# Kernel optimization log

Hardware: AMD Instinct MI355X
Metric: run time of the kernel (lower is better)

The kernel has to match this reference:

```python
import jax, jax.numpy as jnp
import numpy as np

N = 100000   # nodes
E = 1600000  # edges
F_IN = 256   # input features
H = 64       # hidden
C = 40       # classes


def setup_inputs() -> dict:
    key = jax.random.key(0)
    k = jax.random.split(key, 5)
    x = jax.random.normal(k[0], (N, F_IN), dtype=jnp.float32)
    edge_index = jax.random.randint(k[1], (2, E), 0, N, dtype=jnp.int64)
    edge_attr = jax.random.uniform(k[2], (E,), dtype=jnp.float32)
    # GCNConv params (glorot-ish scale), biases zero like reset_parameters
    W1 = jax.random.normal(k[3], (F_IN, H), dtype=jnp.float32) * (1.0 / np.sqrt(F_IN))
    b1 = jnp.zeros((H,), dtype=jnp.float32)
    W2 = jax.random.normal(k[4], (H, C), dtype=jnp.float32) * (1.0 / np.sqrt(H))
    b2 = jnp.zeros((C,), dtype=jnp.float32)
    return {"x": x, "edge_index": edge_index, "edge_attr": edge_attr,
            "W1": W1, "b1": b1, "W2": W2, "b2": b2}


def _gcn_conv(x, W, b, src, dst, norm):
    h = x @ W                                   # [N, out]
    msg = h[src] * norm[:, None]                # gather + edge scale [E+N, out]
    out = jax.ops.segment_sum(msg, dst, num_segments=N)
    return out + b


def reference(x, edge_index, edge_attr, W1, b1, W2, b2):
    # gcn_norm: add self-loops (weight 1), symmetric D^-1/2 A D^-1/2
    loop = jnp.arange(N, dtype=edge_index.dtype)
    src = jnp.concatenate([edge_index[0], loop])
    dst = jnp.concatenate([edge_index[1], loop])
    w = jnp.concatenate([edge_attr, jnp.ones((N,), dtype=edge_attr.dtype)])
    deg = jax.ops.segment_sum(w, dst, num_segments=N)
    dinv = jnp.where(deg > 0, jax.lax.rsqrt(jnp.maximum(deg, 1e-30)), 0.0)
    norm = dinv[src] * w * dinv[dst]

    h = _gcn_conv(x, W1, b1, src, dst, norm)
    h = jax.nn.relu(h)                          # dropout is identity in eval mode
    h = _gcn_conv(h, W2, b2, src, dst, norm)
    return jax.nn.log_softmax(h, axis=1)
```

## Files before the change

### kernel.cpp

```cpp
#include <hip/hip_runtime.h>
#include <math.h>

#define NN   100000
#define NE   1600000
#define FIN  256
#define HID  64
#define NC   40
#define NBKT 391
#define EPB  6250
#define CAP  4608

typedef __attribute__((ext_vector_type(8))) short short8;
typedef __attribute__((ext_vector_type(4))) float float4v;

static __device__ __forceinline__ short f2bf(float f) {
    unsigned u = __float_as_uint(f);
    u += 0x7FFFu + ((u >> 16) & 1u);
    return (short)(u >> 16);
}
static __device__ __forceinline__ float bf2f(unsigned short b) {
    return __uint_as_float((unsigned)b << 16);
}

__global__ __launch_bounds__(256) void w1cvt_k(const float* __restrict__ W1,
                                               short* __restrict__ w1t) {
    int t = blockIdx.x * 256 + threadIdx.x;
    int k = t >> 6, n = t & 63;
    w1t[n * FIN + k] = f2bf(W1[k * HID + n]);
}

__global__ __launch_bounds__(256) void phaseA_k(const int* __restrict__ src,
                                                const int* __restrict__ dst,
                                                const float* __restrict__ w,
                                                int* __restrict__ cursor,
                                                int2* __restrict__ bucketbuf) {
    __shared__ int  hist[NBKT];
    __shared__ int  sc[512];
    __shared__ int  loc_base[NBKT];
    __shared__ int  loc_cur[NBKT];
    __shared__ int  gb[NBKT];
    __shared__ int2 buf[EPB];
    const int t  = threadIdx.x;
    const int e0 = blockIdx.x * EPB;

    for (int i = t; i < NBKT; i += 256) hist[i] = 0;
    __syncthreads();
    for (int i = t; i < EPB; i += 256) atomicAdd(&hist[dst[e0 + i] >> 8], 1);
    __syncthreads();
    sc[t]       = (t       < NBKT) ? hist[t]       : 0;
    sc[t + 256] = (t + 256 < NBKT) ? hist[t + 256] : 0;
    __syncthreads();
    for (int off = 1; off < 512; off <<= 1) {
        int a0 = (t >= off) ? sc[t - off] : 0;
        int a1 = sc[t + 256 - off];
        __syncthreads();
        sc[t] += a0; sc[t + 256] += a1;
        __syncthreads();
    }
    for (int i = t; i < NBKT; i += 256) {
        int base = sc[i] - hist[i];
        loc_base[i] = base;
        loc_cur[i]  = base;
        gb[i] = atomicAdd(&cursor[i * 16], hist[i]);
    }
    __syncthreads();
    for (int i = t; i < EPB; i += 256) {
        int e = e0 + i;
        int d = dst[e];
        int b = d >> 8;
        int p = atomicAdd(&loc_cur[b], 1);
        buf[p] = make_int2(src[e] | ((d & 255) << 17), __float_as_int(w[e]));
    }
    __syncthreads();
    for (int b = t; b < NBKT; b += 256) {
        int lb = loc_base[b], n = hist[b];
        int2* dstp = bucketbuf + (size_t)b * CAP + gb[b];
        for (int i = 0; i < n; ++i) dstp[i] = buf[lb + i];
    }
}

__global__ __launch_bounds__(512) void scanB_k(const int* __restrict__ cursor,
                                               int* __restrict__ bucketbase,
                                               int* __restrict__ row_start) {
    __shared__ int tmp[512];
    int t = threadIdx.x;
    int v = (t < NBKT) ? cursor[t * 16] : 0;
    tmp[t] = v;
    __syncthreads();
    for (int off = 1; off < 512; off <<= 1) {
        int add = (t >= off) ? tmp[t - off] : 0;
        __syncthreads(); tmp[t] += add; __syncthreads();
    }
    if (t < NBKT) bucketbase[t] = tmp[t] - v;
    if (t == 0) { bucketbase[NBKT] = NE; row_start[NN] = NE; }
}

__global__ __launch_bounds__(256) void phaseB_k(const int* __restrict__ bucketbase,
                                                const int2* __restrict__ bucketbuf,
                                                int2* __restrict__ e8,
                                                int* __restrict__ row_start,
                                                float* __restrict__ dinv) {
    __shared__ int2 buf[CAP];
    __shared__ int2 buf2[CAP];
    __shared__ int  hist2[256];
    __shared__ int  tmp[256];
    __shared__ int  base2[257];
    __shared__ int  cur2[256];
    const int b = blockIdx.x, t = threadIdx.x;
    const int g0   = bucketbase[b];
    const int cntb = bucketbase[b + 1] - g0;
    const int n0   = b * 256;
    const int nnb  = (NN - n0 < 256) ? (NN - n0) : 256;

    hist2[t] = 0;
    __syncthreads();
    const int2* bb = bucketbuf + (size_t)b * CAP;
    for (int i = t; i < cntb; i += 256) {
        int2 kv = bb[i];
        buf[i] = kv;
        atomicAdd(&hist2[kv.x >> 17], 1);
    }
    __syncthreads();
    int v = hist2[t];
    tmp[t] = v;
    __syncthreads();
    for (int off = 1; off < 256; off <<= 1) {
        int add = (t >= off) ? tmp[t - off] : 0;
        __syncthreads(); tmp[t] += add; __syncthreads();
    }
    int excl = tmp[t] - v;
    base2[t] = excl;
    cur2[t]  = excl;
    if (t == 0) base2[256] = cntb;
    if (t < nnb) row_start[n0 + t] = g0 + excl;
    __syncthreads();
    for (int i = t; i < cntb; i += 256) {
        int2 kv = buf[i];
        int d = kv.x >> 17;
        int p = atomicAdd(&cur2[d], 1);
        buf2[p] = make_int2(kv.x & 0x1FFFF, kv.y);
    }
    __syncthreads();
    for (int i = t; i < cntb; i += 256) e8[g0 + i] = buf2[i];
    if (t < nnb) {
        float s = 0.f;
        int j1 = base2[t + 1];
        for (int j = base2[t]; j < j1; ++j) s += __int_as_float(buf2[j].y);
        dinv[n0 + t] = rsqrtf(1.0f + s);
    }
}

__global__ __launch_bounds__(256) void gemm1_mfma_k(const float* __restrict__ x,
                                                    const short* __restrict__ w1t,
                                                    unsigned short* __restrict__ h1) {
    const int wave = threadIdx.x >> 6;
    const int lane = threadIdx.x & 63;
    const int m    = lane & 15;
    const int quad = lane >> 4;
    const int r0   = blockIdx.x * 64 + wave * 16;
    const int row  = r0 + m;
    const int rcl  = (row < NN) ? row : (NN - 1);
    const float* xrow = x + (size_t)rcl * FIN + quad * 8;

    float4v acc0 = {0.f,0.f,0.f,0.f}, acc1 = acc0, acc2 = acc0, acc3 = acc0;

#pragma unroll
    for (int kc = 0; kc < 8; ++kc) {
        const int kof = kc * 32 + quad * 8;
        float4 xa = *(const float4*)(xrow + kc * 32);
        float4 xb = *(const float4*)(xrow + kc * 32 + 4);
        short8 a;
        a[0] = f2bf(xa.x); a[1] = f2bf(xa.y); a[2] = f2bf(xa.z); a[3] = f2bf(xa.w);
        a[4] = f2bf(xb.x); a[5] = f2bf(xb.y); a[6] = f2bf(xb.z); a[7] = f2bf(xb.w);
        short8 b0 = *(const short8*)(w1t + (0 * 16 + m) * FIN + kof);
        short8 b1 = *(const short8*)(w1t + (1 * 16 + m) * FIN + kof);
        short8 b2 = *(const short8*)(w1t + (2 * 16 + m) * FIN + kof);
        short8 b3 = *(const short8*)(w1t + (3 * 16 + m) * FIN + kof);
        acc0 = __builtin_amdgcn_mfma_f32_16x16x32_bf16(a, b0, acc0, 0, 0, 0);
        acc1 = __builtin_amdgcn_mfma_f32_16x16x32_bf16(a, b1, acc1, 0, 0, 0);
        acc2 = __builtin_amdgcn_mfma_f32_16x16x32_bf16(a, b2, acc2, 0, 0, 0);
        acc3 = __builtin_amdgcn_mfma_f32_16x16x32_bf16(a, b3, acc3, 0, 0, 0);
    }
#pragma unroll
    for (int r = 0; r < 4; ++r) {
        int rr = r0 + quad * 4 + r;
        if (rr < NN) {
            unsigned short* hp = h1 + (size_t)rr * HID + m;
            hp[0]  = (unsigned short)f2bf(acc0[r]);
            hp[16] = (unsigned short)f2bf(acc1[r]);
            hp[32] = (unsigned short)f2bf(acc2[r]);
            hp[48] = (unsigned short)f2bf(acc3[r]);
        }
    }
}

__global__ __launch_bounds__(256) void gather64_k(const int* __restrict__ row_start,
                                                  const int2* __restrict__ e8,
                                                  const float* __restrict__ dinv,
                                                  const unsigned short* __restrict__ h,
                                                  float* __restrict__ agg) {
    const int v = blockIdx.x * 4 + (threadIdx.x >> 6);
    const int lane = threadIdx.x & 63;
    const int i0 = row_start[v], i1 = row_start[v + 1];
    float acc0 = 0.f, acc1 = 0.f, acc2 = 0.f, acc3 = 0.f;
    int i = i0;
    for (; i + 4 <= i1; i += 4) {
        int2 a = e8[i + 0], b = e8[i + 1], c = e8[i + 2], d = e8[i + 3];
        float wa = dinv[a.x] * __int_as_float(a.y);
        float wb = dinv[b.x] * __int_as_float(b.y);
        float wc = dinv[c.x] * __int_as_float(c.y);
        float wd = dinv[d.x] * __int_as_float(d.y);
        acc0 = fmaf(bf2f(h[(size_t)a.x * HID + lane]), wa, acc0);
        acc1 = fmaf(bf2f(h[(size_t)b.x * HID + lane]), wb, acc1);
        acc2 = fmaf(bf2f(h[(size_t)c.x * HID + lane]), wc, acc2);
        acc3 = fmaf(bf2f(h[(size_t)d.x * HID + lane]), wd, acc3);
    }
    for (; i < i1; ++i) {
        int2 a = e8[i];
        acc0 = fmaf(bf2f(h[(size_t)a.x * HID + lane]), dinv[a.x] * __int_as_float(a.y), acc0);
    }
    const float dv = dinv[v];
    float r = dv * ((acc0 + acc1) + (acc2 + acc3));
    r = fmaf(dv * dv, bf2f(h[(size_t)v * HID + lane]), r);
    agg[(size_t)v * HID + lane] = r;
}

__global__ __launch_bounds__(256) void gemm2_k(const float* __restrict__ agg1,
                                               const float* __restrict__ b1,
                                               const float* __restrict__ W2,
                                               unsigned short* __restrict__ h2) {
    __shared__ float w2s[HID * NC];
    __shared__ float b1s[HID];
    for (int i = threadIdx.x; i < HID * NC; i += 256) w2s[i] = W2[i];
    if (threadIdx.x < HID) b1s[threadIdx.x] = b1[threadIdx.x];
    __syncthreads();

    const int r = blockIdx.x * 256 + threadIdx.x;
    if (r >= NN) return;
    float acc[NC];
#pragma unroll
    for (int c = 0; c < NC; ++c) acc[c] = 0.f;

    const float4* row4 = (const float4*)(agg1 + (size_t)r * HID);
    for (int kk = 0; kk < HID; kk += 4) {
        float4 v = row4[kk >> 2];
        float xr0 = fmaxf(v.x + b1s[kk + 0], 0.f);
        float xr1 = fmaxf(v.y + b1s[kk + 1], 0.f);
        float xr2 = fmaxf(v.z + b1s[kk + 2], 0.f);
        float xr3 = fmaxf(v.w + b1s[kk + 3], 0.f);
#pragma unroll
        for (int c = 0; c < NC; ++c) {
            acc[c] = fmaf(xr0, w2s[(kk + 0) * NC + c], acc[c]);
            acc[c] = fmaf(xr1, w2s[(kk + 1) * NC + c], acc[c]);
            acc[c] = fmaf(xr2, w2s[(kk + 2) * NC + c], acc[c]);
            acc[c] = fmaf(xr3, w2s[(kk + 3) * NC + c], acc[c]);
        }
    }
    unsigned short* outp = h2 + (size_t)r * NC;
    ushort2* o2 = (ushort2*)outp;
#pragma unroll
    for (int c = 0; c < NC; c += 2)
        o2[c >> 1] = make_ushort2((unsigned short)f2bf(acc[c]), (unsigned short)f2bf(acc[c + 1]));
}

__global__ __launch_bounds__(256) void gather40_logsm_k(const int* __restrict__ row_start,
                                                        const int2* __restrict__ e8,
                                                        const float* __restrict__ dinv,
                                                        const unsigned short* __restrict__ h,
                                                        const float* __restrict__ b2,
                                                        float* __restrict__ out) {
    const int v = blockIdx.x * 4 + (threadIdx.x >> 6);
    const int lane = threadIdx.x & 63;
    const int i0 = row_start[v], i1 = row_start[v + 1];
    const int cl = (lane < NC) ? lane : 0;
    float acc0 = 0.f, acc1 = 0.f, acc2 = 0.f, acc3 = 0.f;
    int i = i0;
    for (; i + 4 <= i1; i += 4) {
        int2 a = e8[i + 0], b = e8[i + 1], c = e8[i + 2], d = e8[i + 3];
        float wa = dinv[a.x] * __int_as_float(a.y);
        float wb = dinv[b.x] * __int_as_float(b.y);
        float wc = dinv[c.x] * __int_as_float(c.y);
        float wd = dinv[d.x] * __int_as_float(d.y);
        acc0 = fmaf(bf2f(h[(size_t)a.x * NC + cl]), wa, acc0);
        acc1 = fmaf(bf2f(h[(size_t)b.x * NC + cl]), wb, acc1);
        acc2 = fmaf(bf2f(h[(size_t)c.x * NC + cl]), wc, acc2);
        acc3 = fmaf(bf2f(h[(size_t)d.x * NC + cl]), wd, acc3);
    }
    for (; i < i1; ++i) {
        int2 a = e8[i];
        acc0 = fmaf(bf2f(h[(size_t)a.x * NC + cl]), dinv[a.x] * __int_as_float(a.y), acc0);
    }
    const float dv = dinv[v];
    float vv = dv * ((acc0 + acc1) + (acc2 + acc3));
    vv = fmaf(dv * dv, bf2f(h[(size_t)v * NC + cl]), vv);
    vv += b2[cl];

    float m = (lane < NC) ? vv : -INFINITY;
#pragma unroll
    for (int off = 32; off >= 1; off >>= 1) m = fmaxf(m, __shfl_xor(m, off, 64));
    float ex = (lane < NC) ? __expf(vv - m) : 0.f;
    float s = ex;
#pragma unroll
    for (int off = 32; off >= 1; off >>= 1) s += __shfl_xor(s, off, 64);
    if (lane < NC) out[(size_t)v * NC + lane] = vv - m - __logf(s);
}

extern "C" void kernel_launch(void* const* d_in, const int* in_sizes, int n_in,
                              void* d_out, int out_size, void* d_ws, size_t ws_size,
                              hipStream_t stream) {
    const float* x  = (const float*)d_in[0];
    const int*   ei = (const int*)d_in[1];
    const float* ea = (const float*)d_in[2];
    const float* W1 = (const float*)d_in[3];
    const float* b1 = (const float*)d_in[4];
    const float* W2 = (const float*)d_in[5];
    const float* b2 = (const float*)d_in[6];
    const int* src = ei;
    const int* dst = ei + NE;
    float* out = (float*)d_out;

    char* ws = (char*)d_ws;
    float* dinv       = (float*)(ws + 0);
    int*   row_start  = (int*)  (ws + 400000);
    int*   cursor     = (int*)  (ws + 800016);
    int*   bucketbase = (int*)  (ws + 825040);
    int2*  e8         = (int2*) (ws + 826608);
    unsigned short* h1 = (unsigned short*)(ws + 13626608);
    float* agg1       = (float*)(ws + 26426608);
    short* w1t        = (short*)(ws + 52026608);
    int2*  bucketbuf  = (int2*)agg1;
    unsigned short* h2 = h1;

    hipMemsetAsync(cursor, 0, 391 * 16 * sizeof(int), stream);

    w1cvt_k <<<64,   256, 0, stream>>>(W1, w1t);
    phaseA_k<<<256,  256, 0, stream>>>(src, dst, ea, cursor, bucketbuf);
    scanB_k <<<1,    512, 0, stream>>>(cursor, bucketbase, row_start);
    phaseB_k<<<NBKT, 256, 0, stream>>>(bucketbase, bucketbuf, e8, row_start, dinv);

    gemm1_mfma_k    <<<(NN + 63) / 64, 256, 0, stream>>>(x, w1t, h1);
    gather64_k      <<<NN / 4, 256, 0, stream>>>(row_start, e8, dinv, h1, agg1);
    gemm2_k         <<<(NN + 255) / 256, 256, 0, stream>>>(agg1, b1, W2, h2);
    gather40_logsm_k<<<NN / 4, 256, 0, stream>>>(row_start, e8, dinv, h2, b2, out);
}
```

Before: 431.6 us.

## Pre-scale features by dinv and aggregate before second GEMM

Folds the source-side D^-1/2 scaling into the producer kernels (GEMM1 output and post-ReLU activations), so the edge loops no longer gather dinv per edge. Reorders layer 2 to aggregate the 64-wide hidden features first and then multiply by W2, fusing bias and log-softmax into a per-row GEMM kernel. This removes a random dinv gather per edge in both passes and the separate gemm2 kernel. In exchange the second gather reads 64-wide rows instead of 40-wide ones, writes a float agg2 buffer, and adds a per-thread softmax over 40 registers.

```diff
diff --git a/kernel.cpp b/kernel.cpp
--- a/kernel.cpp
+++ b/kernel.cpp
@@ -152,6 +152,7 @@
 
 __global__ __launch_bounds__(256) void gemm1_mfma_k(const float* __restrict__ x,
                                                     const short* __restrict__ w1t,
+                                                    const float* __restrict__ dinv,
                                                     unsigned short* __restrict__ h1) {
     const int wave = threadIdx.x >> 6;
     const int lane = threadIdx.x & 63;
@@ -185,20 +186,22 @@
     for (int r = 0; r < 4; ++r) {
         int rr = r0 + quad * 4 + r;
         if (rr < NN) {
+            float dv = dinv[rr];
             unsigned short* hp = h1 + (size_t)rr * HID + m;
-            hp[0]  = (unsigned short)f2bf(acc0[r]);
-            hp[16] = (unsigned short)f2bf(acc1[r]);
-            hp[32] = (unsigned short)f2bf(acc2[r]);
-            hp[48] = (unsigned short)f2bf(acc3[r]);
+            hp[0]  = (unsigned short)f2bf(acc0[r] * dv);
+            hp[16] = (unsigned short)f2bf(acc1[r] * dv);
+            hp[32] = (unsigned short)f2bf(acc2[r] * dv);
+            hp[48] = (unsigned short)f2bf(acc3[r] * dv);
         }
     }
 }
 
-__global__ __launch_bounds__(256) void gather64_k(const int* __restrict__ row_start,
-                                                  const int2* __restrict__ e8,
-                                                  const float* __restrict__ dinv,
-                                                  const unsigned short* __restrict__ h,
-                                                  float* __restrict__ agg) {
+__global__ __launch_bounds__(256) void gatherA_k(const int* __restrict__ row_start,
+                                                 const int2* __restrict__ e8,
+                                                 const float* __restrict__ dinv,
+                                                 const unsigned short* __restrict__ h,
+                                                 const float* __restrict__ b1,
+                                                 unsigned short* __restrict__ Rp) {
     const int v = blockIdx.x * 4 + (threadIdx.x >> 6);
     const int lane = threadIdx.x & 63;
     const int i0 = row_start[v], i1 = row_start[v + 1];
@@ -206,103 +209,86 @@
     int i = i0;
     for (; i + 4 <= i1; i += 4) {
         int2 a = e8[i + 0], b = e8[i + 1], c = e8[i + 2], d = e8[i + 3];
-        float wa = dinv[a.x] * __int_as_float(a.y);
-        float wb = dinv[b.x] * __int_as_float(b.y);
-        float wc = dinv[c.x] * __int_as_float(c.y);
-        float wd = dinv[d.x] * __int_as_float(d.y);
-        acc0 = fmaf(bf2f(h[(size_t)a.x * HID + lane]), wa, acc0);
-        acc1 = fmaf(bf2f(h[(size_t)b.x * HID + lane]), wb, acc1);
-        acc2 = fmaf(bf2f(h[(size_t)c.x * HID + lane]), wc, acc2);
-        acc3 = fmaf(bf2f(h[(size_t)d.x * HID + lane]), wd, acc3);
+        acc0 = fmaf(bf2f(h[(size_t)a.x * HID + lane]), __int_as_float(a.y), acc0);
+        acc1 = fmaf(bf2f(h[(size_t)b.x * HID + lane]), __int_as_float(b.y), acc1);
+        acc2 = fmaf(bf2f(h[(size_t)c.x * HID + lane]), __int_as_float(c.y), acc2);
+        acc3 = fmaf(bf2f(h[(size_t)d.x * HID + lane]), __int_as_float(d.y), acc3);
     }
     for (; i < i1; ++i) {
         int2 a = e8[i];
-        acc0 = fmaf(bf2f(h[(size_t)a.x * HID + lane]), dinv[a.x] * __int_as_float(a.y), acc0);
+        acc0 = fmaf(bf2f(h[(size_t)a.x * HID + lane]), __int_as_float(a.y), acc0);
     }
     const float dv = dinv[v];
-    float r = dv * ((acc0 + acc1) + (acc2 + acc3));
-    r = fmaf(dv * dv, bf2f(h[(size_t)v * HID + lane]), r);
-    agg[(size_t)v * HID + lane] = r;
-}
-
-__global__ __launch_bounds__(256) void gemm2_k(const float* __restrict__ agg1,
-                                               const float* __restrict__ b1,
-                                               const float* __restrict__ W2,
-                                               unsigned short* __restrict__ h2) {
-    __shared__ float w2s[HID * NC];
-    __shared__ float b1s[HID];
-    for (int i = threadIdx.x; i < HID * NC; i += 256) w2s[i] = W2[i];
-    if (threadIdx.x < HID) b1s[threadIdx.x] = b1[threadIdx.x];
-    __syncthreads();
-
-    const int r = blockIdx.x * 256 + threadIdx.x;
-    if (r >= NN) return;
-    float acc[NC];
-#pragma unroll
-    for (int c = 0; c < NC; ++c) acc[c] = 0.f;
-
-    const float4* row4 = (const float4*)(agg1 + (size_t)r * HID);
-    for (int kk = 0; kk < HID; kk += 4) {
-        float4 v = row4[kk >> 2];
-        float xr0 = fmaxf(v.x + b1s[kk + 0], 0.f);
-        float xr1 = fmaxf(v.y + b1s[kk + 1], 0.f);
-        float xr2 = fmaxf(v.z + b1s[kk + 2], 0.f);
-        float xr3 = fmaxf(v.w + b1s[kk + 3], 0.f);
-#pragma unroll
-        for (int c = 0; c < NC; ++c) {
-            acc[c] = fmaf(xr0, w2s[(kk + 0) * NC + c], acc[c]);
-            acc[c] = fmaf(xr1, w2s[(kk + 1) * NC + c], acc[c]);
-            acc[c] = fmaf(xr2, w2s[(kk + 2) * NC + c], acc[c]);
-            acc[c] = fmaf(xr3, w2s[(kk + 3) * NC + c], acc[c]);
-        }
-    }
-    unsigned short* outp = h2 + (size_t)r * NC;
-    ushort2* o2 = (ushort2*)outp;
-#pragma unroll
-    for (int c = 0; c < NC; c += 2)
-        o2[c >> 1] = make_ushort2((unsigned short)f2bf(acc[c]), (unsigned short)f2bf(acc[c + 1]));
-}
-
-__global__ __launch_bounds__(256) void gather40_logsm_k(const int* __restrict__ row_start,
-                                                        const int2* __restrict__ e8,
-                                                        const float* __restrict__ dinv,
-                                                        const unsigned short* __restrict__ h,
-                                                        const float* __restrict__ b2,
-                                                        float* __restrict__ out) {
+    float r = (acc0 + acc1) + (acc2 + acc3);
+    r = dv * (r + bf2f(h[(size_t)v * HID + lane]));
+    r = fmaxf(r + b1[lane], 0.f);
+    Rp[(size_t)v * HID + lane] = (unsigned short)f2bf(dv * r);
+}
+
+__global__ __launch_bounds__(256) void gatherB_k(const int* __restrict__ row_start,
+                                                 const int2* __restrict__ e8,
+                                                 const float* __restrict__ dinv,
+                                                 const unsigned short* __restrict__ Rp,
+                                                 float* __restrict__ agg2) {
     const int v = blockIdx.x * 4 + (threadIdx.x >> 6);
     const int lane = threadIdx.x & 63;
     const int i0 = row_start[v], i1 = row_start[v + 1];
-    const int cl = (lane < NC) ? lane : 0;
     float acc0 = 0.f, acc1 = 0.f, acc2 = 0.f, acc3 = 0.f;
     int i = i0;
     for (; i + 4 <= i1; i += 4) {
         int2 a = e8[i + 0], b = e8[i + 1], c = e8[i + 2], d = e8[i + 3];
-        float wa = dinv[a.x] * __int_as_float(a.y);
-        float wb = dinv[b.x] * __int_as_float(b.y);
-        float wc = dinv[c.x] * __int_as_float(c.y);
-        float wd = dinv[d.x] * __int_as_float(d.y);
-        acc0 = fmaf(bf2f(h[(size_t)a.x * NC + cl]), wa, acc0);
-        acc1 = fmaf(bf2f(h[(size_t)b.x * NC + cl]), wb, acc1);
-        acc2 = fmaf(bf2f(h[(size_t)c.x * NC + cl]), wc, acc2);
-        acc3 = fmaf(bf2f(h[(size_t)d.x * NC + cl]), wd, acc3);
+        acc0 = fmaf(bf2f(Rp[(size_t)a.x * HID + lane]), __int_as_float(a.y), acc0);
+        acc1 = fmaf(bf2f(Rp[(size_t)b.x * HID + lane]), __int_as_float(b.y), acc1);
+        acc2 = fmaf(bf2f(Rp[(size_t)c.x * HID + lane]), __int_as_float(c.y), acc2);
+        acc3 = fmaf(bf2f(Rp[(size_t)d.x * HID + lane]), __int_as_float(d.y), acc3);
     }
     for (; i < i1; ++i) {
         int2 a = e8[i];
-        acc0 = fmaf(bf2f(h[(size_t)a.x * NC + cl]), dinv[a.x] * __int_as_float(a.y), acc0);
+        acc0 = fmaf(bf2f(Rp[(size_t)a.x * HID + lane]), __int_as_float(a.y), acc0);
     }
     const float dv = dinv[v];
-    float vv = dv * ((acc0 + acc1) + (acc2 + acc3));
-    vv = fmaf(dv * dv, bf2f(h[(size_t)v * NC + cl]), vv);
-    vv += b2[cl];
-
-    float m = (lane < NC) ? vv : -INFINITY;
-#pragma unroll
-    for (int off = 32; off >= 1; off >>= 1) m = fmaxf(m, __shfl_xor(m, off, 64));
-    float ex = (lane < NC) ? __expf(vv - m) : 0.f;
-    float s = ex;
-#pragma unroll
-    for (int off = 32; off >= 1; off >>= 1) s += __shfl_xor(s, off, 64);
-    if (lane < NC) out[(size_t)v * NC + lane] = vv - m - __logf(s);
+    float r = (acc0 + acc1) + (acc2 + acc3);
+    agg2[(size_t)v * HID + lane] = dv * (r + bf2f(Rp[(size_t)v * HID + lane]));
+}
+
+__global__ __launch_bounds__(256) void gemm3_logsm_k(const float* __restrict__ agg2,
+                                                     const float* __restrict__ W2,
+                                                     const float* __restrict__ b2,
+                                                     float* __restrict__ out) {
+    __shared__ float w2s[HID * NC];
+    __shared__ float b2s[NC];
+    for (int i = threadIdx.x; i < HID * NC; i += 256) w2s[i] = W2[i];
+    if (threadIdx.x < NC) b2s[threadIdx.x] = b2[threadIdx.x];
+    __syncthreads();
+
+    const int r = blockIdx.x * 256 + threadIdx.x;
+    if (r >= NN) return;
+    float acc[NC];
+#pragma unroll
+    for (int c = 0; c < NC; ++c) acc[c] = b2s[c];
+
+    const float4* row4 = (const float4*)(agg2 + (size_t)r * HID);
+    for (int kk = 0; kk < HID; kk += 4) {
+        float4 v = row4[kk >> 2];
+#pragma unroll
+        for (int c = 0; c < NC; ++c) {
+            acc[c] = fmaf(v.x, w2s[(kk + 0) * NC + c], acc[c]);
+            acc[c] = fmaf(v.y, w2s[(kk + 1) * NC + c], acc[c]);
+            acc[c] = fmaf(v.z, w2s[(kk + 2) * NC + c], acc[c]);
+            acc[c] = fmaf(v.w, w2s[(kk + 3) * NC + c], acc[c]);
+        }
+    }
+    float m = acc[0];
+#pragma unroll
+    for (int c = 1; c < NC; ++c) m = fmaxf(m, acc[c]);
+    float s = 0.f;
+#pragma unroll
+    for (int c = 0; c < NC; ++c) s += __expf(acc[c] - m);
+    float lg = m + __logf(s);
+    float* outp = out + (size_t)r * NC;
+#pragma unroll
+    for (int c = 0; c < NC; c += 4)
+        *(float4*)&outp[c] = make_float4(acc[c] - lg, acc[c+1] - lg, acc[c+2] - lg, acc[c+3] - lg);
 }
 
 extern "C" void kernel_launch(void* const* d_in, const int* in_sizes, int n_in,
@@ -326,10 +312,10 @@
     int*   bucketbase = (int*)  (ws + 825040);
     int2*  e8         = (int2*) (ws + 826608);
     unsigned short* h1 = (unsigned short*)(ws + 13626608);
-    float* agg1       = (float*)(ws + 26426608);
-    short* w1t        = (short*)(ws + 52026608);
-    int2*  bucketbuf  = (int2*)agg1;
-    unsigned short* h2 = h1;
+    unsigned short* Rp = (unsigned short*)(ws + 26426608);
+    float* agg2       = (float*)(ws + 39226608);
+    short* w1t        = (short*)(ws + 64826608);
+    int2*  bucketbuf  = (int2*)agg2;
 
     hipMemsetAsync(cursor, 0, 391 * 16 * sizeof(int), stream);
 
@@ -338,8 +324,8 @@
     scanB_k <<<1,    512, 0, stream>>>(cursor, bucketbase, row_start);
     phaseB_k<<<NBKT, 256, 0, stream>>>(bucketbase, bucketbuf, e8, row_start, dinv);
 
-    gemm1_mfma_k    <<<(NN + 63) / 64, 256, 0, stream>>>(x, w1t, h1);
-    gather64_k      <<<NN / 4, 256, 0, stream>>>(row_start, e8, dinv, h1, agg1);
-    gemm2_k         <<<(NN + 255) / 256, 256, 0, stream>>>(agg1, b1, W2, h2);
-    gather40_logsm_k<<<NN / 4, 256, 0, stream>>>(row_start, e8, dinv, h2, b2, out);
-}
+    gemm1_mfma_k <<<(NN + 63) / 64, 256, 0, stream>>>(x, w1t, dinv, h1);
+    gatherA_k    <<<NN / 4, 256, 0, stream>>>(row_start, e8, dinv, h1, b1, Rp);
+    gatherB_k    <<<NN / 4, 256, 0, stream>>>(row_start, e8, dinv, Rp, agg2);
+    gemm3_logsm_k<<<(NN + 255) / 256, 256, 0, stream>>>(agg2, W2, b2, out);
+}
```

Result: faster. 419.9 us (-2.7%).
